# Performance work log

Hardware: AMD Instinct MI355X
Metric: run time of the kernel (lower is better)

Reference implementation:

```python
import jax, jax.numpy as jnp
import numpy as np

B, C, N, D, S = 512, 256, 2048, 64, 3

def setup_inputs() -> dict:
    key = jax.random.key(0)
    k1, k2, k3, k4, k5 = jax.random.split(key, 5)
    controller_output = jax.random.normal(k1, (B, C), dtype=jnp.float32)
    w_prev = jax.random.uniform(k2, (B, N), dtype=jnp.float32)
    w_prev = w_prev / jnp.sum(w_prev, axis=-1, keepdims=True)  # valid attention weighting
    M_t = jax.random.normal(k3, (B, N, D), dtype=jnp.float32)
    emit_len = D + 1 + 1 + S + 1  # read_split sum = 70
    W = jax.random.normal(k4, (C, emit_len), dtype=jnp.float32) * (1.0 / np.sqrt(C))
    b = jax.random.normal(k5, (emit_len,), dtype=jnp.float32) * 0.05
    return {"controller_output": controller_output, "w_t_1": w_prev, "M_t": M_t, "W": W, "b": b}

def reference(controller_output, w_t_1, M_t, W, b):
    # fc_addr: Dense with tanh activation
    fc = jnp.tanh(controller_output @ W + b)  # [B, 70]
    # split per read_split [D,1,1,S,1] and apply emit activations
    k_t = fc[:, :D]                                            # [B, D] (already tanh'd)
    beta_t = jax.nn.softplus(fc[:, D:D + 1])                   # [B, 1] key strength
    g_t = jax.nn.sigmoid(fc[:, D + 1:D + 2])                   # [B, 1] interpolation gate
    s_t = jax.nn.softmax(fc[:, D + 2:D + 2 + S], axis=-1)      # [B, S] shift weighting
    gamma_t = 1.0 + jax.nn.softplus(fc[:, D + 2 + S:D + 3 + S])  # [B, 1] sharpen
    # content addressing: cosine similarity (no epsilon, faithful to source)
    dot = jnp.einsum('bd,bnd->bn', k_t, M_t)                   # [B, N]
    k_mag = jnp.sqrt(jnp.sum(k_t * k_t, axis=-1, keepdims=True))  # [B, 1]
    m_mag = jnp.sqrt(jnp.sum(M_t * M_t, axis=-1))              # [B, N]
    cos = dot / (k_mag * m_mag)
    w_c_t = jax.nn.softmax(beta_t * cos, axis=-1)              # [B, N]
    # interpolation
    w_g_t = g_t * w_c_t + (1.0 - g_t) * w_t_1                  # [B, N]
    # circular convolution shift: sum_i roll(w, i - S//2) * s[:, i]
    w_tilde = jnp.zeros_like(w_g_t)
    for i in range(S):
        w_tilde = w_tilde + jnp.roll(w_g_t, i - S // 2, axis=-1) * s_t[:, i:i + 1]
    # sharpening
    w_raised = jnp.power(w_tilde, gamma_t)
    w_t = w_raised / jnp.sum(w_raised, axis=-1, keepdims=True)  # [B, N]
    # read
    r_t = jnp.einsum('bn,bnd->bd', w_t, M_t)                   # [B, D]
    return (r_t, w_t)
```

## Files before the change

kernel.cpp:

```cpp
#include <hip/hip_runtime.h>
#include <math.h>

constexpr int Bb = 512;
constexpr int Cc = 256;
constexpr int Nn = 2048;
constexpr int Dd = 64;
constexpr int EMIT = Dd + 1 + 1 + 3 + 1;
constexpr int BLOCK = 1024;
constexpr int NW = BLOCK / 64;

__global__ __launch_bounds__(BLOCK, 8)
void ntm_read_head_kernel(const float* __restrict__ co,
                          const float* __restrict__ wprev,
                          const float* __restrict__ M,
                          const float* __restrict__ W,
                          const float* __restrict__ bias,
                          float* __restrict__ out_r,
                          float* __restrict__ out_w)
{
    const int b    = blockIdx.x;
    const int t    = threadIdx.x;
    const int lane = t & 63;
    const int wv   = t >> 6;

    __shared__ __align__(16) float fc[EMIT + 2];
    __shared__ float sc[8];
    __shared__ __align__(16) float zbuf[Nn];
    __shared__ float wpbuf[Nn];
    __shared__ float wtbuf[Nn];
    __shared__ float redA[NW], redB[NW];
    __shared__ float rred[NW][Dd];

    {
        const float* wpv = wprev + (size_t)b * Nn;
        wpbuf[t]        = wpv[t];
        wpbuf[t + 1024] = wpv[t + 1024];
    }

    const float* corow = co + (size_t)b * Cc;
    {
        float* fcp = zbuf;
        if (t < 980) {
            const int j    = t % EMIT;
            const int part = t / EMIT;
            const int c0 = part * 19;
            const int c1 = (c0 + 19 < Cc) ? c0 + 19 : Cc;
            float s = 0.f;
            for (int c = c0; c < c1; ++c)
                s = fmaf(corow[c], W[(size_t)c * EMIT + j], s);
            fcp[part * EMIT + j] = s;
        }
        __syncthreads();
        if (t < EMIT) {
            float s = bias[t];
            #pragma unroll
            for (int w = 0; w < 14; ++w) s += fcp[w * EMIT + t];
            fc[t] = tanhf(s);
        }
    }
    __syncthreads();

    if (t < 64) {
        float kk  = fc[t];
        float ksq = kk * kk;
        #pragma unroll
        for (int o = 1; o < 64; o <<= 1) ksq += __shfl_xor(ksq, o);
        if (t == 0) {
            float kmag  = sqrtf(ksq);
            float beta  = log1pf(expf(fc[Dd]));
            float g     = 1.f / (1.f + expf(-fc[Dd + 1]));
            float f0 = fc[Dd + 2], f1 = fc[Dd + 3], f2 = fc[Dd + 4];
            float mx = fmaxf(f0, fmaxf(f1, f2));
            float e0 = expf(f0 - mx), e1 = expf(f1 - mx), e2 = expf(f2 - mx);
            float ei = 1.f / (e0 + e1 + e2);
            float gamma = 1.f + log1pf(expf(fc[Dd + 5]));
            sc[0] = beta; sc[1] = g;
            sc[2] = e0 * ei; sc[3] = e1 * ei; sc[4] = e2 * ei;
            sc[5] = gamma; sc[6] = 1.f / kmag;
        }
    }
    __syncthreads();

    const size_t mbase = (size_t)b * Nn * Dd;
    float lmax = -3.4e38f;
    {
        const int rg = t >> 2;
        const int p  = t & 3;
        const float beta = sc[0];
        const float kinv = sc[6];
        const float4 k0 = *(const float4*)&fc[p * 16 + 0];
        const float4 k1 = *(const float4*)&fc[p * 16 + 4];
        const float4 k2 = *(const float4*)&fc[p * 16 + 8];
        const float4 k3 = *(const float4*)&fc[p * 16 + 12];
        for (int n0 = 0; n0 < Nn; n0 += BLOCK / 4) {
            const int n = n0 + rg;
            const float4* mr = (const float4*)&M[mbase + (size_t)n * Dd + p * 16];
            const float4 m0 = mr[0];
            const float4 m1 = mr[1];
            const float4 m2 = mr[2];
            const float4 m3 = mr[3];
            float dot = m0.x*k0.x + m0.y*k0.y + m0.z*k0.z + m0.w*k0.w
                      + m1.x*k1.x + m1.y*k1.y + m1.z*k1.z + m1.w*k1.w
                      + m2.x*k2.x + m2.y*k2.y + m2.z*k2.z + m2.w*k2.w
                      + m3.x*k3.x + m3.y*k3.y + m3.z*k3.z + m3.w*k3.w;
            float msq = m0.x*m0.x + m0.y*m0.y + m0.z*m0.z + m0.w*m0.w
                      + m1.x*m1.x + m1.y*m1.y + m1.z*m1.z + m1.w*m1.w
                      + m2.x*m2.x + m2.y*m2.y + m2.z*m2.z + m2.w*m2.w
                      + m3.x*m3.x + m3.y*m3.y + m3.z*m3.z + m3.w*m3.w;
            dot += __shfl_xor(dot, 1);
            msq += __shfl_xor(msq, 1);
            dot += __shfl_xor(dot, 2);
            msq += __shfl_xor(msq, 2);
            if (p == 0) {
                float z = beta * dot * kinv / sqrtf(msq);
                zbuf[n] = z;
                lmax = fmaxf(lmax, z);
            }
        }
    }
    #pragma unroll
    for (int o = 1; o < 64; o <<= 1) lmax = fmaxf(lmax, __shfl_xor(lmax, o));
    if (lane == 0) redA[wv] = lmax;
    __syncthreads();

    float zmax = redA[0];
    #pragma unroll
    for (int w = 1; w < NW; ++w) zmax = fmaxf(zmax, redA[w]);

    float ls = 0.f;
    #pragma unroll
    for (int k = 0; k < 2; ++k) {
        const int n = t + k * 1024;
        float e = __expf(zbuf[n] - zmax);
        zbuf[n] = e;
        ls += e;
    }
    #pragma unroll
    for (int o = 1; o < 64; o <<= 1) ls += __shfl_xor(ls, o);
    if (lane == 0) redB[wv] = ls;
    __syncthreads();

    float Zs = 0.f;
    #pragma unroll
    for (int w = 0; w < NW; ++w) Zs += redB[w];

    float lsum = 0.f;
    {
        const float g  = sc[1];
        const float A  = g / Zs;
        const float Cg = 1.f - g;
        const float s0 = sc[2], s1 = sc[3], s2 = sc[4], gamma = sc[5];
        #pragma unroll
        for (int k = 0; k < 2; ++k) {
            const int n  = t + k * 1024;
            const int np = (n + 1) & (Nn - 1);
            const int nm = (n - 1) & (Nn - 1);
            float ce = s0 * zbuf[np] + s1 * zbuf[n] + s2 * zbuf[nm];
            float cp = s0 * wpbuf[np] + s1 * wpbuf[n] + s2 * wpbuf[nm];
            float wr = __powf(A * ce + Cg * cp, gamma);
            wtbuf[n] = wr;
            lsum += wr;
        }
    }
    #pragma unroll
    for (int o = 1; o < 64; o <<= 1) lsum += __shfl_xor(lsum, o);
    if (lane == 0) redA[wv] = lsum;
    __syncthreads();
    float Ws = 0.f;
    #pragma unroll
    for (int w = 0; w < NW; ++w) Ws += redA[w];

    {
        const float inv = 1.f / Ws;
        float* ow = out_w + (size_t)b * Nn;
        #pragma unroll
        for (int k = 0; k < 2; ++k) {
            const int n = t + k * 1024;
            float v = wtbuf[n] * inv;
            wtbuf[n] = v;
            ow[n] = v;
        }
    }
    __syncthreads();

    {
        const int grp = t >> 4;
        const int dk  = t & 15;
        float4 acc = make_float4(0.f, 0.f, 0.f, 0.f);
        #pragma unroll 4
        for (int n = grp; n < Nn; n += BLOCK / 16) {
            const float w = wtbuf[n];
            const float4 m = *(const float4*)&M[mbase + (size_t)n * Dd + dk * 4];
            acc.x += w * m.x; acc.y += w * m.y;
            acc.z += w * m.z; acc.w += w * m.w;
        }
        #pragma unroll
        for (int o = 16; o < 64; o <<= 1) {
            acc.x += __shfl_xor(acc.x, o);
            acc.y += __shfl_xor(acc.y, o);
            acc.z += __shfl_xor(acc.z, o);
            acc.w += __shfl_xor(acc.w, o);
        }
        if (lane < 16) {
            rred[wv][lane * 4 + 0] = acc.x;
            rred[wv][lane * 4 + 1] = acc.y;
            rred[wv][lane * 4 + 2] = acc.z;
            rred[wv][lane * 4 + 3] = acc.w;
        }
    }
    __syncthreads();
    if (t < Dd) {
        float r = 0.f;
        #pragma unroll
        for (int w = 0; w < NW; ++w) r += rred[w][t];
        out_r[(size_t)b * Dd + t] = r;
    }
}

extern "C" void kernel_launch(void* const* d_in, const int* in_sizes, int n_in,
                              void* d_out, int out_size, void* d_ws, size_t ws_size,
                              hipStream_t stream) {
    const float* co    = (const float*)d_in[0];
    const float* wprev = (const float*)d_in[1];
    const float* M     = (const float*)d_in[2];
    const float* W     = (const float*)d_in[3];
    const float* bias  = (const float*)d_in[4];
    float* out = (float*)d_out;
    float* out_r = out;
    float* out_w = out + (size_t)Bb * Dd;

    ntm_read_head_kernel<<<Bb, BLOCK, 0, stream>>>(co, wprev, M, W, bias, out_r, out_w);
}
```

Baseline: 91.91 us.

## Split fused NTM read head into four kernels staged through workspace

```diff
diff --git a/kernel.cpp b/kernel.cpp
--- a/kernel.cpp
+++ b/kernel.cpp
@@ -6,162 +6,167 @@
 constexpr int Nn = 2048;
 constexpr int Dd = 64;
 constexpr int EMIT = Dd + 1 + 1 + 3 + 1;
-constexpr int BLOCK = 1024;
-constexpr int NW = BLOCK / 64;
-
-__global__ __launch_bounds__(BLOCK, 8)
-void ntm_read_head_kernel(const float* __restrict__ co,
-                          const float* __restrict__ wprev,
-                          const float* __restrict__ M,
-                          const float* __restrict__ W,
-                          const float* __restrict__ bias,
-                          float* __restrict__ out_r,
-                          float* __restrict__ out_w)
-{
-    const int b    = blockIdx.x;
-    const int t    = threadIdx.x;
-    const int lane = t & 63;
-    const int wv   = t >> 6;
-
-    __shared__ __align__(16) float fc[EMIT + 2];
-    __shared__ float sc[8];
-    __shared__ __align__(16) float zbuf[Nn];
+constexpr int NW = 16;
+
+constexpr int FC_STRIDE = 80;
+constexpr int Z_OFF     = Bb * FC_STRIDE;
+constexpr int ZMAX_OFF  = Z_OFF + Bb * Nn;
+
+__global__ __launch_bounds__(256)
+void k0_fc(const float* __restrict__ co, const float* __restrict__ W,
+           const float* __restrict__ bias, float* __restrict__ ws)
+{
+    const int b = blockIdx.x, t = threadIdx.x;
+    __shared__ float part[3][EMIT];
+    __shared__ float fcrow[EMIT];
+    const float* corow = co + (size_t)b * Cc;
+
+    if (t < 210) {
+        const int j = t % EMIT, p = t / EMIT;
+        const int c0 = p * 86, c1 = (p == 2) ? Cc : c0 + 86;
+        float s = 0.f;
+        for (int c = c0; c < c1; ++c)
+            s = fmaf(corow[c], W[(size_t)c * EMIT + j], s);
+        part[p][j] = s;
+    }
+    __syncthreads();
+    if (t < EMIT)
+        fcrow[t] = tanhf(bias[t] + part[0][t] + part[1][t] + part[2][t]);
+    __syncthreads();
+
+    float* wsrow = ws + (size_t)b * FC_STRIDE;
+    if (t < 64) {
+        float kk = fcrow[t];
+        wsrow[t] = kk;
+        float ksq = kk * kk;
+        #pragma unroll
+        for (int o = 1; o < 64; o <<= 1) ksq += __shfl_xor(ksq, o);
+        if (t == 0) {
+            float kinv  = 1.f / sqrtf(ksq);
+            float beta  = log1pf(expf(fcrow[Dd]));
+            float g     = 1.f / (1.f + expf(-fcrow[Dd + 1]));
+            float f0 = fcrow[Dd + 2], f1 = fcrow[Dd + 3], f2 = fcrow[Dd + 4];
+            float mx = fmaxf(f0, fmaxf(f1, f2));
+            float e0 = expf(f0 - mx), e1 = expf(f1 - mx), e2 = expf(f2 - mx);
+            float ei = 1.f / (e0 + e1 + e2);
+            float gamma = 1.f + log1pf(expf(fcrow[Dd + 5]));
+            wsrow[64] = beta; wsrow[65] = g;
+            wsrow[66] = e0 * ei; wsrow[67] = e1 * ei; wsrow[68] = e2 * ei;
+            wsrow[69] = gamma; wsrow[70] = kinv;
+        }
+    }
+}
+
+__global__ __launch_bounds__(1024, 8)
+void k1a_cos(const float* __restrict__ M, float* __restrict__ ws)
+{
+    const int b = blockIdx.x, t = threadIdx.x;
+    const int lane = t & 63, wv = t >> 6;
+    __shared__ __align__(16) float kf[72];
+    __shared__ float redA[NW];
+
+    if (t < 72) kf[t] = ws[(size_t)b * FC_STRIDE + t];
+    __syncthreads();
+
+    const float bk = kf[64] * kf[70];
+    const int rg = t >> 2, p = t & 3;
+    const float4 k0 = *(const float4*)&kf[p * 16 + 0];
+    const float4 k1 = *(const float4*)&kf[p * 16 + 4];
+    const float4 k2 = *(const float4*)&kf[p * 16 + 8];
+    const float4 k3 = *(const float4*)&kf[p * 16 + 12];
+
+    const size_t mbase = (size_t)b * Nn * Dd;
+    float* zrow = ws + Z_OFF + (size_t)b * Nn;
+    float lmax = -3.4e38f;
+
+    #pragma unroll 2
+    for (int n0 = 0; n0 < Nn; n0 += 256) {
+        const int n = n0 + rg;
+        const float4* mr = (const float4*)&M[mbase + (size_t)n * Dd + p * 16];
+        const float4 m0 = mr[0], m1 = mr[1], m2 = mr[2], m3 = mr[3];
+        float dot = m0.x*k0.x + m0.y*k0.y + m0.z*k0.z + m0.w*k0.w
+                  + m1.x*k1.x + m1.y*k1.y + m1.z*k1.z + m1.w*k1.w
+                  + m2.x*k2.x + m2.y*k2.y + m2.z*k2.z + m2.w*k2.w
+                  + m3.x*k3.x + m3.y*k3.y + m3.z*k3.z + m3.w*k3.w;
+        float msq = m0.x*m0.x + m0.y*m0.y + m0.z*m0.z + m0.w*m0.w
+                  + m1.x*m1.x + m1.y*m1.y + m1.z*m1.z + m1.w*m1.w
+                  + m2.x*m2.x + m2.y*m2.y + m2.z*m2.z + m2.w*m2.w
+                  + m3.x*m3.x + m3.y*m3.y + m3.z*m3.z + m3.w*m3.w;
+        dot += __shfl_xor(dot, 1);
+        msq += __shfl_xor(msq, 1);
+        dot += __shfl_xor(dot, 2);
+        msq += __shfl_xor(msq, 2);
+        if (p == 0) {
+            float z = bk * dot / sqrtf(msq);
+            zrow[n] = z;
+            lmax = fmaxf(lmax, z);
+        }
+    }
+    #pragma unroll
+    for (int o = 1; o < 64; o <<= 1) lmax = fmaxf(lmax, __shfl_xor(lmax, o));
+    if (lane == 0) redA[wv] = lmax;
+    __syncthreads();
+    if (t == 0) {
+        float zmax = redA[0];
+        #pragma unroll
+        for (int w = 1; w < NW; ++w) zmax = fmaxf(zmax, redA[w]);
+        ws[ZMAX_OFF + b] = zmax;
+    }
+}
+
+__global__ __launch_bounds__(1024, 8)
+void k1b_weights(const float* __restrict__ wprev, float* __restrict__ ws,
+                 float* __restrict__ out_w)
+{
+    const int b = blockIdx.x, t = threadIdx.x;
+    const int lane = t & 63, wv = t >> 6;
+    __shared__ float zbuf[Nn];
     __shared__ float wpbuf[Nn];
-    __shared__ float wtbuf[Nn];
+    __shared__ float kf[72];
     __shared__ float redA[NW], redB[NW];
-    __shared__ float rred[NW][Dd];
-
+
+    if (t < 72) kf[t] = ws[(size_t)b * FC_STRIDE + t];
     {
         const float* wpv = wprev + (size_t)b * Nn;
         wpbuf[t]        = wpv[t];
         wpbuf[t + 1024] = wpv[t + 1024];
     }
-
-    const float* corow = co + (size_t)b * Cc;
-    {
-        float* fcp = zbuf;
-        if (t < 980) {
-            const int j    = t % EMIT;
-            const int part = t / EMIT;
-            const int c0 = part * 19;
-            const int c1 = (c0 + 19 < Cc) ? c0 + 19 : Cc;
-            float s = 0.f;
-            for (int c = c0; c < c1; ++c)
-                s = fmaf(corow[c], W[(size_t)c * EMIT + j], s);
-            fcp[part * EMIT + j] = s;
-        }
-        __syncthreads();
-        if (t < EMIT) {
-            float s = bias[t];
-            #pragma unroll
-            for (int w = 0; w < 14; ++w) s += fcp[w * EMIT + t];
-            fc[t] = tanhf(s);
-        }
-    }
-    __syncthreads();
-
-    if (t < 64) {
-        float kk  = fc[t];
-        float ksq = kk * kk;
-        #pragma unroll
-        for (int o = 1; o < 64; o <<= 1) ksq += __shfl_xor(ksq, o);
-        if (t == 0) {
-            float kmag  = sqrtf(ksq);
-            float beta  = log1pf(expf(fc[Dd]));
-            float g     = 1.f / (1.f + expf(-fc[Dd + 1]));
-            float f0 = fc[Dd + 2], f1 = fc[Dd + 3], f2 = fc[Dd + 4];
-            float mx = fmaxf(f0, fmaxf(f1, f2));
-            float e0 = expf(f0 - mx), e1 = expf(f1 - mx), e2 = expf(f2 - mx);
-            float ei = 1.f / (e0 + e1 + e2);
-            float gamma = 1.f + log1pf(expf(fc[Dd + 5]));
-            sc[0] = beta; sc[1] = g;
-            sc[2] = e0 * ei; sc[3] = e1 * ei; sc[4] = e2 * ei;
-            sc[5] = gamma; sc[6] = 1.f / kmag;
-        }
-    }
-    __syncthreads();
-
-    const size_t mbase = (size_t)b * Nn * Dd;
-    float lmax = -3.4e38f;
-    {
-        const int rg = t >> 2;
-        const int p  = t & 3;
-        const float beta = sc[0];
-        const float kinv = sc[6];
-        const float4 k0 = *(const float4*)&fc[p * 16 + 0];
-        const float4 k1 = *(const float4*)&fc[p * 16 + 4];
-        const float4 k2 = *(const float4*)&fc[p * 16 + 8];
-        const float4 k3 = *(const float4*)&fc[p * 16 + 12];
-        for (int n0 = 0; n0 < Nn; n0 += BLOCK / 4) {
-            const int n = n0 + rg;
-            const float4* mr = (const float4*)&M[mbase + (size_t)n * Dd + p * 16];
-            const float4 m0 = mr[0];
-            const float4 m1 = mr[1];
-            const float4 m2 = mr[2];
-            const float4 m3 = mr[3];
-            float dot = m0.x*k0.x + m0.y*k0.y + m0.z*k0.z + m0.w*k0.w
-                      + m1.x*k1.x + m1.y*k1.y + m1.z*k1.z + m1.w*k1.w
-                      + m2.x*k2.x + m2.y*k2.y + m2.z*k2.z + m2.w*k2.w
-                      + m3.x*k3.x + m3.y*k3.y + m3.z*k3.z + m3.w*k3.w;
-            float msq = m0.x*m0.x + m0.y*m0.y + m0.z*m0.z + m0.w*m0.w
-                      + m1.x*m1.x + m1.y*m1.y + m1.z*m1.z + m1.w*m1.w
-                      + m2.x*m2.x + m2.y*m2.y + m2.z*m2.z + m2.w*m2.w
-                      + m3.x*m3.x + m3.y*m3.y + m3.z*m3.z + m3.w*m3.w;
-            dot += __shfl_xor(dot, 1);
-            msq += __shfl_xor(msq, 1);
-            dot += __shfl_xor(dot, 2);
-            msq += __shfl_xor(msq, 2);
-            if (p == 0) {
-                float z = beta * dot * kinv / sqrtf(msq);
-                zbuf[n] = z;
-                lmax = fmaxf(lmax, z);
-            }
-        }
-    }
-    #pragma unroll
-    for (int o = 1; o < 64; o <<= 1) lmax = fmaxf(lmax, __shfl_xor(lmax, o));
-    if (lane == 0) redA[wv] = lmax;
-    __syncthreads();
-
-    float zmax = redA[0];
-    #pragma unroll
-    for (int w = 1; w < NW; ++w) zmax = fmaxf(zmax, redA[w]);
+    const float zmax = ws[ZMAX_OFF + b];
+    const float* zrow = ws + Z_OFF + (size_t)b * Nn;
 
     float ls = 0.f;
-    #pragma unroll
-    for (int k = 0; k < 2; ++k) {
-        const int n = t + k * 1024;
-        float e = __expf(zbuf[n] - zmax);
-        zbuf[n] = e;
-        ls += e;
-    }
+    float e0_ = __expf(zrow[t] - zmax);
+    float e1_ = __expf(zrow[t + 1024] - zmax);
+    ls = e0_ + e1_;
+    __syncthreads();
+    zbuf[t] = e0_;
+    zbuf[t + 1024] = e1_;
     #pragma unroll
     for (int o = 1; o < 64; o <<= 1) ls += __shfl_xor(ls, o);
     if (lane == 0) redB[wv] = ls;
     __syncthreads();
-
     float Zs = 0.f;
     #pragma unroll
     for (int w = 0; w < NW; ++w) Zs += redB[w];
 
-    float lsum = 0.f;
+    const float g  = kf[65];
+    const float A  = g / Zs;
+    const float Cg = 1.f - g;
+    const float s0 = kf[66], s1 = kf[67], s2 = kf[68], gamma = kf[69];
+    float wr0, wr1, lsum;
     {
-        const float g  = sc[1];
-        const float A  = g / Zs;
-        const float Cg = 1.f - g;
-        const float s0 = sc[2], s1 = sc[3], s2 = sc[4], gamma = sc[5];
-        #pragma unroll
-        for (int k = 0; k < 2; ++k) {
-            const int n  = t + k * 1024;
-            const int np = (n + 1) & (Nn - 1);
-            const int nm = (n - 1) & (Nn - 1);
-            float ce = s0 * zbuf[np] + s1 * zbuf[n] + s2 * zbuf[nm];
-            float cp = s0 * wpbuf[np] + s1 * wpbuf[n] + s2 * wpbuf[nm];
-            float wr = __powf(A * ce + Cg * cp, gamma);
-            wtbuf[n] = wr;
-            lsum += wr;
-        }
-    }
+        const int n  = t;
+        const int np = (n + 1) & (Nn - 1), nm = (n - 1) & (Nn - 1);
+        wr0 = __powf(A * (s0 * zbuf[np] + s1 * zbuf[n] + s2 * zbuf[nm])
+                   + Cg * (s0 * wpbuf[np] + s1 * wpbuf[n] + s2 * wpbuf[nm]), gamma);
+    }
+    {
+        const int n  = t + 1024;
+        const int np = (n + 1) & (Nn - 1), nm = (n - 1) & (Nn - 1);
+        wr1 = __powf(A * (s0 * zbuf[np] + s1 * zbuf[n] + s2 * zbuf[nm])
+                   + Cg * (s0 * wpbuf[np] + s1 * wpbuf[n] + s2 * wpbuf[nm]), gamma);
+    }
+    lsum = wr0 + wr1;
     #pragma unroll
     for (int o = 1; o < 64; o <<= 1) lsum += __shfl_xor(lsum, o);
     if (lane == 0) redA[wv] = lsum;
@@ -170,43 +175,50 @@
     #pragma unroll
     for (int w = 0; w < NW; ++w) Ws += redA[w];
 
-    {
-        const float inv = 1.f / Ws;
-        float* ow = out_w + (size_t)b * Nn;
-        #pragma unroll
-        for (int k = 0; k < 2; ++k) {
-            const int n = t + k * 1024;
-            float v = wtbuf[n] * inv;
-            wtbuf[n] = v;
-            ow[n] = v;
-        }
-    }
-    __syncthreads();
-
-    {
-        const int grp = t >> 4;
-        const int dk  = t & 15;
-        float4 acc = make_float4(0.f, 0.f, 0.f, 0.f);
-        #pragma unroll 4
-        for (int n = grp; n < Nn; n += BLOCK / 16) {
-            const float w = wtbuf[n];
-            const float4 m = *(const float4*)&M[mbase + (size_t)n * Dd + dk * 4];
-            acc.x += w * m.x; acc.y += w * m.y;
-            acc.z += w * m.z; acc.w += w * m.w;
-        }
-        #pragma unroll
-        for (int o = 16; o < 64; o <<= 1) {
-            acc.x += __shfl_xor(acc.x, o);
-            acc.y += __shfl_xor(acc.y, o);
-            acc.z += __shfl_xor(acc.z, o);
-            acc.w += __shfl_xor(acc.w, o);
-        }
-        if (lane < 16) {
-            rred[wv][lane * 4 + 0] = acc.x;
-            rred[wv][lane * 4 + 1] = acc.y;
-            rred[wv][lane * 4 + 2] = acc.z;
-            rred[wv][lane * 4 + 3] = acc.w;
-        }
+    const float inv = 1.f / Ws;
+    float* ow = out_w + (size_t)b * Nn;
+    ow[t]        = wr0 * inv;
+    ow[t + 1024] = wr1 * inv;
+}
+
+__global__ __launch_bounds__(1024, 8)
+void k2_read(const float* __restrict__ M, const float* __restrict__ out_w,
+             float* __restrict__ out_r)
+{
+    const int b = blockIdx.x, t = threadIdx.x;
+    const int lane = t & 63, wv = t >> 6;
+    __shared__ float wtbuf[Nn];
+    __shared__ float rred[NW][Dd];
+
+    const float* wrow = out_w + (size_t)b * Nn;
+    wtbuf[t]        = wrow[t];
+    wtbuf[t + 1024] = wrow[t + 1024];
+    __syncthreads();
+
+    const size_t mbase = (size_t)b * Nn * Dd;
+    const int grp = t >> 4;
+    const int dk  = t & 15;
+    float4 acc = make_float4(0.f, 0.f, 0.f, 0.f);
+    #pragma unroll 4
+    for (int i = 0; i < Nn / 64; ++i) {
+        const int n = (Nn - 64) - i * 64 + grp;
+        const float w = wtbuf[n];
+        const float4 m = *(const float4*)&M[mbase + (size_t)n * Dd + dk * 4];
+        acc.x += w * m.x; acc.y += w * m.y;
+        acc.z += w * m.z; acc.w += w * m.w;
+    }
+    #pragma unroll
+    for (int o = 16; o < 64; o <<= 1) {
+        acc.x += __shfl_xor(acc.x, o);
+        acc.y += __shfl_xor(acc.y, o);
+        acc.z += __shfl_xor(acc.z, o);
+        acc.w += __shfl_xor(acc.w, o);
+    }
+    if (lane < 16) {
+        rred[wv][lane * 4 + 0] = acc.x;
+        rred[wv][lane * 4 + 1] = acc.y;
+        rred[wv][lane * 4 + 2] = acc.z;
+        rred[wv][lane * 4 + 3] = acc.w;
     }
     __syncthreads();
     if (t < Dd) {
@@ -225,9 +237,13 @@
     const float* M     = (const float*)d_in[2];
     const float* W     = (const float*)d_in[3];
     const float* bias  = (const float*)d_in[4];
-    float* out = (float*)d_out;
+    float* out   = (float*)d_out;
     float* out_r = out;
     float* out_w = out + (size_t)Bb * Dd;
-
-    ntm_read_head_kernel<<<Bb, BLOCK, 0, stream>>>(co, wprev, M, W, bias, out_r, out_w);
-}
+    float* ws    = (float*)d_ws;
+
+    k0_fc      <<<Bb, 256,  0, stream>>>(co, W, bias, ws);
+    k1a_cos    <<<Bb, 1024, 0, stream>>>(M, ws);
+    k1b_weights<<<Bb, 1024, 0, stream>>>(wprev, ws, out_w);
+    k2_read    <<<Bb, 1024, 0, stream>>>(M, out_w, out_r);
+}
```

After: 133.4 us. +45.1%, slower.

## Process two batch rows per block, overlapping row0 read with row1 scoring

Applied to the files above, without the earlier changes.

```diff
diff --git a/kernel.cpp b/kernel.cpp
--- a/kernel.cpp
+++ b/kernel.cpp
@@ -8,8 +8,9 @@
 constexpr int EMIT = Dd + 1 + 1 + 3 + 1;
 constexpr int BLOCK = 1024;
 constexpr int NW = BLOCK / 64;
-
-__global__ __launch_bounds__(BLOCK, 8)
+constexpr int GRID = Bb / 2;
+
+__global__ __launch_bounds__(BLOCK, 4)
 void ntm_read_head_kernel(const float* __restrict__ co,
                           const float* __restrict__ wprev,
                           const float* __restrict__ M,
@@ -18,87 +19,98 @@
                           float* __restrict__ out_r,
                           float* __restrict__ out_w)
 {
-    const int b    = blockIdx.x;
+    const int r0 = blockIdx.x * 2;
+    const int r1 = r0 + 1;
     const int t    = threadIdx.x;
     const int lane = t & 63;
     const int wv   = t >> 6;
 
-    __shared__ __align__(16) float fc[EMIT + 2];
-    __shared__ float sc[8];
-    __shared__ __align__(16) float zbuf[Nn];
-    __shared__ float wpbuf[Nn];
-    __shared__ float wtbuf[Nn];
+    __shared__ __align__(16) float fc0[72], fc1[72];
+    __shared__ __align__(16) float zbuf0[Nn], zbuf1[Nn];
+    __shared__ float wp0[Nn], wp1[Nn];
+    __shared__ float wt0[Nn], wt1[Nn];
     __shared__ float redA[NW], redB[NW];
     __shared__ float rred[NW][Dd];
 
     {
-        const float* wpv = wprev + (size_t)b * Nn;
-        wpbuf[t]        = wpv[t];
-        wpbuf[t + 1024] = wpv[t + 1024];
-    }
-
-    const float* corow = co + (size_t)b * Cc;
-    {
-        float* fcp = zbuf;
+        const float* a = wprev + (size_t)r0 * Nn;
+        const float* b = wprev + (size_t)r1 * Nn;
+        wp0[t] = a[t];  wp0[t + 1024] = a[t + 1024];
+        wp1[t] = b[t];  wp1[t + 1024] = b[t + 1024];
+    }
+
+    {
+        const float* co0 = co + (size_t)r0 * Cc;
+        const float* co1 = co + (size_t)r1 * Cc;
         if (t < 980) {
-            const int j    = t % EMIT;
-            const int part = t / EMIT;
+            const int j = t % EMIT, part = t / EMIT;
             const int c0 = part * 19;
             const int c1 = (c0 + 19 < Cc) ? c0 + 19 : Cc;
-            float s = 0.f;
-            for (int c = c0; c < c1; ++c)
-                s = fmaf(corow[c], W[(size_t)c * EMIT + j], s);
-            fcp[part * EMIT + j] = s;
+            float sA = 0.f, sB = 0.f;
+            for (int c = c0; c < c1; ++c) {
+                const float w = W[(size_t)c * EMIT + j];
+                sA = fmaf(co0[c], w, sA);
+                sB = fmaf(co1[c], w, sB);
+            }
+            zbuf0[part * EMIT + j] = sA;
+            zbuf1[part * EMIT + j] = sB;
         }
         __syncthreads();
         if (t < EMIT) {
             float s = bias[t];
             #pragma unroll
-            for (int w = 0; w < 14; ++w) s += fcp[w * EMIT + t];
-            fc[t] = tanhf(s);
-        }
-    }
-    __syncthreads();
-
-    if (t < 64) {
-        float kk  = fc[t];
+            for (int w = 0; w < 14; ++w) s += zbuf0[w * EMIT + t];
+            fc0[t] = tanhf(s);
+        } else if (t >= 512 && t < 512 + EMIT) {
+            const int j = t - 512;
+            float s = bias[j];
+            #pragma unroll
+            for (int w = 0; w < 14; ++w) s += zbuf1[w * EMIT + j];
+            fc1[j] = tanhf(s);
+        }
+        __syncthreads();
+    }
+
+    if (t < 128) {
+        float* fcX = (t < 64) ? fc0 : fc1;
+        const int l = t & 63;
+        float kk  = fcX[l];
         float ksq = kk * kk;
         #pragma unroll
         for (int o = 1; o < 64; o <<= 1) ksq += __shfl_xor(ksq, o);
-        if (t == 0) {
-            float kmag  = sqrtf(ksq);
-            float beta  = log1pf(expf(fc[Dd]));
-            float g     = 1.f / (1.f + expf(-fc[Dd + 1]));
-            float f0 = fc[Dd + 2], f1 = fc[Dd + 3], f2 = fc[Dd + 4];
+        if (l == 0) {
+            float kinv  = 1.f / sqrtf(ksq);
+            float beta  = log1pf(expf(fcX[Dd]));
+            float g     = 1.f / (1.f + expf(-fcX[Dd + 1]));
+            float f0 = fcX[Dd + 2], f1 = fcX[Dd + 3], f2 = fcX[Dd + 4];
             float mx = fmaxf(f0, fmaxf(f1, f2));
             float e0 = expf(f0 - mx), e1 = expf(f1 - mx), e2 = expf(f2 - mx);
             float ei = 1.f / (e0 + e1 + e2);
-            float gamma = 1.f + log1pf(expf(fc[Dd + 5]));
-            sc[0] = beta; sc[1] = g;
-            sc[2] = e0 * ei; sc[3] = e1 * ei; sc[4] = e2 * ei;
-            sc[5] = gamma; sc[6] = 1.f / kmag;
-        }
-    }
-    __syncthreads();
-
-    const size_t mbase = (size_t)b * Nn * Dd;
-    float lmax = -3.4e38f;
-    {
-        const int rg = t >> 2;
-        const int p  = t & 3;
-        const float beta = sc[0];
-        const float kinv = sc[6];
-        const float4 k0 = *(const float4*)&fc[p * 16 + 0];
-        const float4 k1 = *(const float4*)&fc[p * 16 + 4];
-        const float4 k2 = *(const float4*)&fc[p * 16 + 8];
-        const float4 k3 = *(const float4*)&fc[p * 16 + 12];
-        for (int n0 = 0; n0 < Nn; n0 += BLOCK / 4) {
+            float gamma = 1.f + log1pf(expf(fcX[Dd + 5]));
+            fcX[64] = beta; fcX[65] = g;
+            fcX[66] = e0 * ei; fcX[67] = e1 * ei; fcX[68] = e2 * ei;
+            fcX[69] = gamma; fcX[70] = kinv;
+        }
+    }
+    __syncthreads();
+
+    const size_t mb0 = (size_t)r0 * Nn * Dd;
+    const size_t mb1 = (size_t)r1 * Nn * Dd;
+    const int rg = t >> 2, p = t & 3;
+    const int grp = t >> 4, dk = t & 15;
+
+    float lmax0 = -3.4e38f;
+    {
+        const float bk = fc0[64] * fc0[70];
+        const float4 k0 = *(const float4*)&fc0[p * 16 + 0];
+        const float4 k1 = *(const float4*)&fc0[p * 16 + 4];
+        const float4 k2 = *(const float4*)&fc0[p * 16 + 8];
+        const float4 k3 = *(const float4*)&fc0[p * 16 + 12];
+        #pragma unroll 2
+        for (int n0 = 0; n0 < Nn; n0 += 256) {
             const int n = n0 + rg;
-            const float4* mr = (const float4*)&M[mbase + (size_t)n * Dd + p * 16];
-            const float4 m0 = mr[0];
-            const float4 m1 = mr[1];
-            const float4 m2 = mr[2];
-            const float4 m3 = mr[3];
+            const float4* mr = (const float4*)&M[mb0 + (size_t)n * Dd + p * 16];
+            const float4 m0 = mr[0], m1 = mr[1], m2 = mr[2], m3 = mr[3];
             float dot = m0.x*k0.x + m0.y*k0.y + m0.z*k0.z + m0.w*k0.w
                       + m1.x*k1.x + m1.y*k1.y + m1.z*k1.z + m1.w*k1.w
                       + m2.x*k2.x + m2.y*k2.y + m2.z*k2.z + m2.w*k2.w
@@ -107,90 +119,180 @@
                       + m1.x*m1.x + m1.y*m1.y + m1.z*m1.z + m1.w*m1.w
                       + m2.x*m2.x + m2.y*m2.y + m2.z*m2.z + m2.w*m2.w
                       + m3.x*m3.x + m3.y*m3.y + m3.z*m3.z + m3.w*m3.w;
-            dot += __shfl_xor(dot, 1);
-            msq += __shfl_xor(msq, 1);
-            dot += __shfl_xor(dot, 2);
-            msq += __shfl_xor(msq, 2);
+            dot += __shfl_xor(dot, 1);  msq += __shfl_xor(msq, 1);
+            dot += __shfl_xor(dot, 2);  msq += __shfl_xor(msq, 2);
             if (p == 0) {
-                float z = beta * dot * kinv / sqrtf(msq);
-                zbuf[n] = z;
-                lmax = fmaxf(lmax, z);
+                float z = bk * dot / sqrtf(msq);
+                zbuf0[n] = z;
+                lmax0 = fmaxf(lmax0, z);
             }
         }
     }
     #pragma unroll
-    for (int o = 1; o < 64; o <<= 1) lmax = fmaxf(lmax, __shfl_xor(lmax, o));
-    if (lane == 0) redA[wv] = lmax;
-    __syncthreads();
-
-    float zmax = redA[0];
-    #pragma unroll
-    for (int w = 1; w < NW; ++w) zmax = fmaxf(zmax, redA[w]);
-
-    float ls = 0.f;
-    #pragma unroll
-    for (int k = 0; k < 2; ++k) {
-        const int n = t + k * 1024;
-        float e = __expf(zbuf[n] - zmax);
-        zbuf[n] = e;
-        ls += e;
-    }
-    #pragma unroll
-    for (int o = 1; o < 64; o <<= 1) ls += __shfl_xor(ls, o);
-    if (lane == 0) redB[wv] = ls;
-    __syncthreads();
-
-    float Zs = 0.f;
-    #pragma unroll
-    for (int w = 0; w < NW; ++w) Zs += redB[w];
-
-    float lsum = 0.f;
-    {
-        const float g  = sc[1];
-        const float A  = g / Zs;
-        const float Cg = 1.f - g;
-        const float s0 = sc[2], s1 = sc[3], s2 = sc[4], gamma = sc[5];
-        #pragma unroll
-        for (int k = 0; k < 2; ++k) {
-            const int n  = t + k * 1024;
-            const int np = (n + 1) & (Nn - 1);
-            const int nm = (n - 1) & (Nn - 1);
-            float ce = s0 * zbuf[np] + s1 * zbuf[n] + s2 * zbuf[nm];
-            float cp = s0 * wpbuf[np] + s1 * wpbuf[n] + s2 * wpbuf[nm];
-            float wr = __powf(A * ce + Cg * cp, gamma);
-            wtbuf[n] = wr;
-            lsum += wr;
-        }
-    }
-    #pragma unroll
-    for (int o = 1; o < 64; o <<= 1) lsum += __shfl_xor(lsum, o);
-    if (lane == 0) redA[wv] = lsum;
-    __syncthreads();
-    float Ws = 0.f;
-    #pragma unroll
-    for (int w = 0; w < NW; ++w) Ws += redA[w];
-
-    {
+    for (int o = 1; o < 64; o <<= 1) lmax0 = fmaxf(lmax0, __shfl_xor(lmax0, o));
+    if (lane == 0) redA[wv] = lmax0;
+    __syncthreads();
+    float zmax0 = redA[0];
+    #pragma unroll
+    for (int w = 1; w < NW; ++w) zmax0 = fmaxf(zmax0, redA[w]);
+
+    {
+        float e0 = __expf(zbuf0[t] - zmax0);
+        float e1 = __expf(zbuf0[t + 1024] - zmax0);
+        float ls = e0 + e1;
+        zbuf0[t] = e0; zbuf0[t + 1024] = e1;
+        #pragma unroll
+        for (int o = 1; o < 64; o <<= 1) ls += __shfl_xor(ls, o);
+        if (lane == 0) redB[wv] = ls;
+    }
+    __syncthreads();
+    {
+        float Zs = 0.f;
+        #pragma unroll
+        for (int w = 0; w < NW; ++w) Zs += redB[w];
+        const float g  = fc0[65];
+        const float A  = g / Zs, Cg = 1.f - g;
+        const float s0 = fc0[66], s1 = fc0[67], s2 = fc0[68], gamma = fc0[69];
+        float wr0, wr1;
+        {
+            const int n = t, np = (n + 1) & (Nn - 1), nm = (n - 1) & (Nn - 1);
+            wr0 = __powf(A * (s0 * zbuf0[np] + s1 * zbuf0[n] + s2 * zbuf0[nm])
+                       + Cg * (s0 * wp0[np] + s1 * wp0[n] + s2 * wp0[nm]), gamma);
+        }
+        {
+            const int n = t + 1024, np = (n + 1) & (Nn - 1), nm = (n - 1) & (Nn - 1);
+            wr1 = __powf(A * (s0 * zbuf0[np] + s1 * zbuf0[n] + s2 * zbuf0[nm])
+                       + Cg * (s0 * wp0[np] + s1 * wp0[n] + s2 * wp0[nm]), gamma);
+        }
+        float lsum = wr0 + wr1;
+        #pragma unroll
+        for (int o = 1; o < 64; o <<= 1) lsum += __shfl_xor(lsum, o);
+        if (lane == 0) redA[wv] = lsum;
+        __syncthreads();
+        float Ws = 0.f;
+        #pragma unroll
+        for (int w = 0; w < NW; ++w) Ws += redA[w];
         const float inv = 1.f / Ws;
-        float* ow = out_w + (size_t)b * Nn;
-        #pragma unroll
-        for (int k = 0; k < 2; ++k) {
-            const int n = t + k * 1024;
-            float v = wtbuf[n] * inv;
-            wtbuf[n] = v;
-            ow[n] = v;
-        }
-    }
-    __syncthreads();
-
-    {
-        const int grp = t >> 4;
-        const int dk  = t & 15;
+        float* ow = out_w + (size_t)r0 * Nn;
+        wt0[t] = wr0 * inv;        ow[t] = wr0 * inv;
+        wt0[t + 1024] = wr1 * inv; ow[t + 1024] = wr1 * inv;
+    }
+    __syncthreads();
+
+    float lmax1 = -3.4e38f;
+    float4 acc0 = make_float4(0.f, 0.f, 0.f, 0.f);
+    {
+        const float bk = fc1[64] * fc1[70];
+        const float4 k0 = *(const float4*)&fc1[p * 16 + 0];
+        const float4 k1 = *(const float4*)&fc1[p * 16 + 4];
+        const float4 k2 = *(const float4*)&fc1[p * 16 + 8];
+        const float4 k3 = *(const float4*)&fc1[p * 16 + 12];
+        for (int i = 0; i < 8; ++i) {
+            const int n = i * 256 + rg;
+            const float4* mr = (const float4*)&M[mb1 + (size_t)n * Dd + p * 16];
+            const float4 m0 = mr[0], m1 = mr[1], m2 = mr[2], m3 = mr[3];
+            #pragma unroll
+            for (int jj = 0; jj < 4; ++jj) {
+                const int n2 = i * 256 + jj * 64 + grp;
+                const float w = wt0[n2];
+                const float4 mm = *(const float4*)&M[mb0 + (size_t)n2 * Dd + dk * 4];
+                acc0.x += w * mm.x; acc0.y += w * mm.y;
+                acc0.z += w * mm.z; acc0.w += w * mm.w;
+            }
+            float dot = m0.x*k0.x + m0.y*k0.y + m0.z*k0.z + m0.w*k0.w
+                      + m1.x*k1.x + m1.y*k1.y + m1.z*k1.z + m1.w*k1.w
+                      + m2.x*k2.x + m2.y*k2.y + m2.z*k2.z + m2.w*k2.w
+                      + m3.x*k3.x + m3.y*k3.y + m3.z*k3.z + m3.w*k3.w;
+            float msq = m0.x*m0.x + m0.y*m0.y + m0.z*m0.z + m0.w*m0.w
+                      + m1.x*m1.x + m1.y*m1.y + m1.z*m1.z + m1.w*m1.w
+                      + m2.x*m2.x + m2.y*m2.y + m2.z*m2.z + m2.w*m2.w
+                      + m3.x*m3.x + m3.y*m3.y + m3.z*m3.z + m3.w*m3.w;
+            dot += __shfl_xor(dot, 1);  msq += __shfl_xor(msq, 1);
+            dot += __shfl_xor(dot, 2);  msq += __shfl_xor(msq, 2);
+            if (p == 0) {
+                float z = bk * dot / sqrtf(msq);
+                zbuf1[n] = z;
+                lmax1 = fmaxf(lmax1, z);
+            }
+        }
+    }
+    #pragma unroll
+    for (int o = 1; o < 64; o <<= 1) lmax1 = fmaxf(lmax1, __shfl_xor(lmax1, o));
+    if (lane == 0) redA[wv] = lmax1;
+    #pragma unroll
+    for (int o = 16; o < 64; o <<= 1) {
+        acc0.x += __shfl_xor(acc0.x, o);
+        acc0.y += __shfl_xor(acc0.y, o);
+        acc0.z += __shfl_xor(acc0.z, o);
+        acc0.w += __shfl_xor(acc0.w, o);
+    }
+    if (lane < 16) {
+        rred[wv][lane * 4 + 0] = acc0.x;
+        rred[wv][lane * 4 + 1] = acc0.y;
+        rred[wv][lane * 4 + 2] = acc0.z;
+        rred[wv][lane * 4 + 3] = acc0.w;
+    }
+    __syncthreads();
+    if (t < Dd) {
+        float r = 0.f;
+        #pragma unroll
+        for (int w = 0; w < NW; ++w) r += rred[w][t];
+        out_r[(size_t)r0 * Dd + t] = r;
+    }
+    float zmax1 = redA[0];
+    #pragma unroll
+    for (int w = 1; w < NW; ++w) zmax1 = fmaxf(zmax1, redA[w]);
+
+    {
+        float e0 = __expf(zbuf1[t] - zmax1);
+        float e1 = __expf(zbuf1[t + 1024] - zmax1);
+        float ls = e0 + e1;
+        zbuf1[t] = e0; zbuf1[t + 1024] = e1;
+        #pragma unroll
+        for (int o = 1; o < 64; o <<= 1) ls += __shfl_xor(ls, o);
+        if (lane == 0) redB[wv] = ls;
+    }
+    __syncthreads();
+    {
+        float Zs = 0.f;
+        #pragma unroll
+        for (int w = 0; w < NW; ++w) Zs += redB[w];
+        const float g  = fc1[65];
+        const float A  = g / Zs, Cg = 1.f - g;
+        const float s0 = fc1[66], s1 = fc1[67], s2 = fc1[68], gamma = fc1[69];
+        float wr0, wr1;
+        {
+            const int n = t, np = (n + 1) & (Nn - 1), nm = (n - 1) & (Nn - 1);
+            wr0 = __powf(A * (s0 * zbuf1[np] + s1 * zbuf1[n] + s2 * zbuf1[nm])
+                       + Cg * (s0 * wp1[np] + s1 * wp1[n] + s2 * wp1[nm]), gamma);
+        }
+        {
+            const int n = t + 1024, np = (n + 1) & (Nn - 1), nm = (n - 1) & (Nn - 1);
+            wr1 = __powf(A * (s0 * zbuf1[np] + s1 * zbuf1[n] + s2 * zbuf1[nm])
+                       + Cg * (s0 * wp1[np] + s1 * wp1[n] + s2 * wp1[nm]), gamma);
+        }
+        float lsum = wr0 + wr1;
+        #pragma unroll
+        for (int o = 1; o < 64; o <<= 1) lsum += __shfl_xor(lsum, o);
+        if (lane == 0) redA[wv] = lsum;
+        __syncthreads();
+        float Ws = 0.f;
+        #pragma unroll
+        for (int w = 0; w < NW; ++w) Ws += redA[w];
+        const float inv = 1.f / Ws;
+        float* ow = out_w + (size_t)r1 * Nn;
+        wt1[t] = wr0 * inv;        ow[t] = wr0 * inv;
+        wt1[t + 1024] = wr1 * inv; ow[t + 1024] = wr1 * inv;
+    }
+    __syncthreads();
+
+    {
         float4 acc = make_float4(0.f, 0.f, 0.f, 0.f);
         #pragma unroll 4
-        for (int n = grp; n < Nn; n += BLOCK / 16) {
-            const float w = wtbuf[n];
-            const float4 m = *(const float4*)&M[mbase + (size_t)n * Dd + dk * 4];
+        for (int i = 0; i < Nn / 64; ++i) {
+            const int n = (Nn - 64) - i * 64 + grp;
+            const float w = wt1[n];
+            const float4 m = *(const float4*)&M[mb1 + (size_t)n * Dd + dk * 4];
             acc.x += w * m.x; acc.y += w * m.y;
             acc.z += w * m.z; acc.w += w * m.w;
         }
@@ -213,7 +315,7 @@
         float r = 0.f;
         #pragma unroll
         for (int w = 0; w < NW; ++w) r += rred[w][t];
-        out_r[(size_t)b * Dd + t] = r;
+        out_r[(size_t)r1 * Dd + t] = r;
     }
 }
 
@@ -225,9 +327,9 @@
     const float* M     = (const float*)d_in[2];
     const float* W     = (const float*)d_in[3];
     const float* bias  = (const float*)d_in[4];
-    float* out = (float*)d_out;
+    float* out   = (float*)d_out;
     float* out_r = out;
     float* out_w = out + (size_t)Bb * Dd;
 
-    ntm_read_head_kernel<<<Bb, BLOCK, 0, stream>>>(co, wprev, M, W, bias, out_r, out_w);
+    ntm_read_head_kernel<<<GRID, BLOCK, 0, stream>>>(co, wprev, M, W, bias, out_r, out_w);
 }
```

After: 131.8 us. +43.5%, slower.

## Split read-head kernel into weight and read kernels, reverse M traversal

Applied to the files above, without the earlier changes.

```diff
diff --git a/kernel.cpp b/kernel.cpp
--- a/kernel.cpp
+++ b/kernel.cpp
@@ -10,26 +10,22 @@
 constexpr int NW = BLOCK / 64;
 
 __global__ __launch_bounds__(BLOCK, 8)
-void ntm_read_head_kernel(const float* __restrict__ co,
-                          const float* __restrict__ wprev,
-                          const float* __restrict__ M,
-                          const float* __restrict__ W,
-                          const float* __restrict__ bias,
-                          float* __restrict__ out_r,
-                          float* __restrict__ out_w)
+void kA_weights(const float* __restrict__ co,
+                const float* __restrict__ wprev,
+                const float* __restrict__ M,
+                const float* __restrict__ W,
+                const float* __restrict__ bias,
+                float* __restrict__ out_w)
 {
     const int b    = blockIdx.x;
     const int t    = threadIdx.x;
     const int lane = t & 63;
     const int wv   = t >> 6;
 
-    __shared__ __align__(16) float fc[EMIT + 2];
-    __shared__ float sc[8];
+    __shared__ __align__(16) float fc[72];
     __shared__ __align__(16) float zbuf[Nn];
     __shared__ float wpbuf[Nn];
-    __shared__ float wtbuf[Nn];
     __shared__ float redA[NW], redB[NW];
-    __shared__ float rred[NW][Dd];
 
     {
         const float* wpv = wprev + (size_t)b * Nn;
@@ -39,22 +35,20 @@
 
     const float* corow = co + (size_t)b * Cc;
     {
-        float* fcp = zbuf;
         if (t < 980) {
-            const int j    = t % EMIT;
-            const int part = t / EMIT;
+            const int j = t % EMIT, part = t / EMIT;
             const int c0 = part * 19;
             const int c1 = (c0 + 19 < Cc) ? c0 + 19 : Cc;
             float s = 0.f;
             for (int c = c0; c < c1; ++c)
                 s = fmaf(corow[c], W[(size_t)c * EMIT + j], s);
-            fcp[part * EMIT + j] = s;
+            zbuf[part * EMIT + j] = s;
         }
         __syncthreads();
         if (t < EMIT) {
             float s = bias[t];
             #pragma unroll
-            for (int w = 0; w < 14; ++w) s += fcp[w * EMIT + t];
+            for (int w = 0; w < 14; ++w) s += zbuf[w * EMIT + t];
             fc[t] = tanhf(s);
         }
     }
@@ -66,7 +60,7 @@
         #pragma unroll
         for (int o = 1; o < 64; o <<= 1) ksq += __shfl_xor(ksq, o);
         if (t == 0) {
-            float kmag  = sqrtf(ksq);
+            float kinv  = 1.f / sqrtf(ksq);
             float beta  = log1pf(expf(fc[Dd]));
             float g     = 1.f / (1.f + expf(-fc[Dd + 1]));
             float f0 = fc[Dd + 2], f1 = fc[Dd + 3], f2 = fc[Dd + 4];
@@ -74,9 +68,9 @@
             float e0 = expf(f0 - mx), e1 = expf(f1 - mx), e2 = expf(f2 - mx);
             float ei = 1.f / (e0 + e1 + e2);
             float gamma = 1.f + log1pf(expf(fc[Dd + 5]));
-            sc[0] = beta; sc[1] = g;
-            sc[2] = e0 * ei; sc[3] = e1 * ei; sc[4] = e2 * ei;
-            sc[5] = gamma; sc[6] = 1.f / kmag;
+            fc[64] = beta; fc[65] = g;
+            fc[66] = e0 * ei; fc[67] = e1 * ei; fc[68] = e2 * ei;
+            fc[69] = gamma; fc[70] = kinv;
         }
     }
     __syncthreads();
@@ -84,21 +78,17 @@
     const size_t mbase = (size_t)b * Nn * Dd;
     float lmax = -3.4e38f;
     {
-        const int rg = t >> 2;
-        const int p  = t & 3;
-        const float beta = sc[0];
-        const float kinv = sc[6];
+        const int rg = t >> 2, p = t & 3;
+        const float bk = fc[64] * fc[70];
         const float4 k0 = *(const float4*)&fc[p * 16 + 0];
         const float4 k1 = *(const float4*)&fc[p * 16 + 4];
         const float4 k2 = *(const float4*)&fc[p * 16 + 8];
         const float4 k3 = *(const float4*)&fc[p * 16 + 12];
-        for (int n0 = 0; n0 < Nn; n0 += BLOCK / 4) {
+        #pragma unroll 2
+        for (int n0 = 0; n0 < Nn; n0 += 256) {
             const int n = n0 + rg;
             const float4* mr = (const float4*)&M[mbase + (size_t)n * Dd + p * 16];
-            const float4 m0 = mr[0];
-            const float4 m1 = mr[1];
-            const float4 m2 = mr[2];
-            const float4 m3 = mr[3];
+            const float4 m0 = mr[0], m1 = mr[1], m2 = mr[2], m3 = mr[3];
             float dot = m0.x*k0.x + m0.y*k0.y + m0.z*k0.z + m0.w*k0.w
                       + m1.x*k1.x + m1.y*k1.y + m1.z*k1.z + m1.w*k1.w
                       + m2.x*k2.x + m2.y*k2.y + m2.z*k2.z + m2.w*k2.w
@@ -107,12 +97,10 @@
                       + m1.x*m1.x + m1.y*m1.y + m1.z*m1.z + m1.w*m1.w
                       + m2.x*m2.x + m2.y*m2.y + m2.z*m2.z + m2.w*m2.w
                       + m3.x*m3.x + m3.y*m3.y + m3.z*m3.z + m3.w*m3.w;
-            dot += __shfl_xor(dot, 1);
-            msq += __shfl_xor(msq, 1);
-            dot += __shfl_xor(dot, 2);
-            msq += __shfl_xor(msq, 2);
+            dot += __shfl_xor(dot, 1);  msq += __shfl_xor(msq, 1);
+            dot += __shfl_xor(dot, 2);  msq += __shfl_xor(msq, 2);
             if (p == 0) {
-                float z = beta * dot * kinv / sqrtf(msq);
+                float z = bk * dot / sqrtf(msq);
                 zbuf[n] = z;
                 lmax = fmaxf(lmax, z);
             }
@@ -122,46 +110,40 @@
     for (int o = 1; o < 64; o <<= 1) lmax = fmaxf(lmax, __shfl_xor(lmax, o));
     if (lane == 0) redA[wv] = lmax;
     __syncthreads();
-
     float zmax = redA[0];
     #pragma unroll
     for (int w = 1; w < NW; ++w) zmax = fmaxf(zmax, redA[w]);
 
-    float ls = 0.f;
-    #pragma unroll
-    for (int k = 0; k < 2; ++k) {
-        const int n = t + k * 1024;
-        float e = __expf(zbuf[n] - zmax);
-        zbuf[n] = e;
-        ls += e;
+    float ls;
+    {
+        float e0 = __expf(zbuf[t] - zmax);
+        float e1 = __expf(zbuf[t + 1024] - zmax);
+        ls = e0 + e1;
+        zbuf[t] = e0; zbuf[t + 1024] = e1;
     }
     #pragma unroll
     for (int o = 1; o < 64; o <<= 1) ls += __shfl_xor(ls, o);
     if (lane == 0) redB[wv] = ls;
     __syncthreads();
-
     float Zs = 0.f;
     #pragma unroll
     for (int w = 0; w < NW; ++w) Zs += redB[w];
 
-    float lsum = 0.f;
-    {
-        const float g  = sc[1];
-        const float A  = g / Zs;
-        const float Cg = 1.f - g;
-        const float s0 = sc[2], s1 = sc[3], s2 = sc[4], gamma = sc[5];
-        #pragma unroll
-        for (int k = 0; k < 2; ++k) {
-            const int n  = t + k * 1024;
-            const int np = (n + 1) & (Nn - 1);
-            const int nm = (n - 1) & (Nn - 1);
-            float ce = s0 * zbuf[np] + s1 * zbuf[n] + s2 * zbuf[nm];
-            float cp = s0 * wpbuf[np] + s1 * wpbuf[n] + s2 * wpbuf[nm];
-            float wr = __powf(A * ce + Cg * cp, gamma);
-            wtbuf[n] = wr;
-            lsum += wr;
-        }
-    }
+    const float g  = fc[65];
+    const float A  = g / Zs, Cg = 1.f - g;
+    const float s0 = fc[66], s1 = fc[67], s2 = fc[68], gamma = fc[69];
+    float wr0, wr1;
+    {
+        const int n = t, np = (n + 1) & (Nn - 1), nm = (n - 1) & (Nn - 1);
+        wr0 = __powf(A * (s0 * zbuf[np] + s1 * zbuf[n] + s2 * zbuf[nm])
+                   + Cg * (s0 * wpbuf[np] + s1 * wpbuf[n] + s2 * wpbuf[nm]), gamma);
+    }
+    {
+        const int n = t + 1024, np = (n + 1) & (Nn - 1), nm = (n - 1) & (Nn - 1);
+        wr1 = __powf(A * (s0 * zbuf[np] + s1 * zbuf[n] + s2 * zbuf[nm])
+                   + Cg * (s0 * wpbuf[np] + s1 * wpbuf[n] + s2 * wpbuf[nm]), gamma);
+    }
+    float lsum = wr0 + wr1;
     #pragma unroll
     for (int o = 1; o < 64; o <<= 1) lsum += __shfl_xor(lsum, o);
     if (lane == 0) redA[wv] = lsum;
@@ -170,43 +152,50 @@
     #pragma unroll
     for (int w = 0; w < NW; ++w) Ws += redA[w];
 
-    {
-        const float inv = 1.f / Ws;
-        float* ow = out_w + (size_t)b * Nn;
-        #pragma unroll
-        for (int k = 0; k < 2; ++k) {
-            const int n = t + k * 1024;
-            float v = wtbuf[n] * inv;
-            wtbuf[n] = v;
-            ow[n] = v;
-        }
-    }
-    __syncthreads();
-
-    {
-        const int grp = t >> 4;
-        const int dk  = t & 15;
-        float4 acc = make_float4(0.f, 0.f, 0.f, 0.f);
-        #pragma unroll 4
-        for (int n = grp; n < Nn; n += BLOCK / 16) {
-            const float w = wtbuf[n];
-            const float4 m = *(const float4*)&M[mbase + (size_t)n * Dd + dk * 4];
-            acc.x += w * m.x; acc.y += w * m.y;
-            acc.z += w * m.z; acc.w += w * m.w;
-        }
-        #pragma unroll
-        for (int o = 16; o < 64; o <<= 1) {
-            acc.x += __shfl_xor(acc.x, o);
-            acc.y += __shfl_xor(acc.y, o);
-            acc.z += __shfl_xor(acc.z, o);
-            acc.w += __shfl_xor(acc.w, o);
-        }
-        if (lane < 16) {
-            rred[wv][lane * 4 + 0] = acc.x;
-            rred[wv][lane * 4 + 1] = acc.y;
-            rred[wv][lane * 4 + 2] = acc.z;
-            rred[wv][lane * 4 + 3] = acc.w;
-        }
+    const float inv = 1.f / Ws;
+    float* ow = out_w + (size_t)b * Nn;
+    ow[t]        = wr0 * inv;
+    ow[t + 1024] = wr1 * inv;
+}
+
+__global__ __launch_bounds__(BLOCK, 8)
+void kB_read(const float* __restrict__ M, const float* __restrict__ out_w,
+             float* __restrict__ out_r)
+{
+    const int b = blockIdx.x, t = threadIdx.x;
+    const int lane = t & 63, wv = t >> 6;
+    __shared__ float wtbuf[Nn];
+    __shared__ float rred[NW][Dd];
+
+    const float* wrow = out_w + (size_t)b * Nn;
+    wtbuf[t]        = wrow[t];
+    wtbuf[t + 1024] = wrow[t + 1024];
+    __syncthreads();
+
+    const size_t mbase = (size_t)b * Nn * Dd;
+    const int grp = t >> 4;
+    const int dk  = t & 15;
+    float4 acc = make_float4(0.f, 0.f, 0.f, 0.f);
+    #pragma unroll 4
+    for (int i = 0; i < Nn / 64; ++i) {
+        const int n = (Nn - 64) - i * 64 + grp;
+        const float w = wtbuf[n];
+        const float4 m = *(const float4*)&M[mbase + (size_t)n * Dd + dk * 4];
+        acc.x += w * m.x; acc.y += w * m.y;
+        acc.z += w * m.z; acc.w += w * m.w;
+    }
+    #pragma unroll
+    for (int o = 16; o < 64; o <<= 1) {
+        acc.x += __shfl_xor(acc.x, o);
+        acc.y += __shfl_xor(acc.y, o);
+        acc.z += __shfl_xor(acc.z, o);
+        acc.w += __shfl_xor(acc.w, o);
+    }
+    if (lane < 16) {
+        rred[wv][lane * 4 + 0] = acc.x;
+        rred[wv][lane * 4 + 1] = acc.y;
+        rred[wv][lane * 4 + 2] = acc.z;
+        rred[wv][lane * 4 + 3] = acc.w;
     }
     __syncthreads();
     if (t < Dd) {
@@ -225,9 +214,10 @@
     const float* M     = (const float*)d_in[2];
     const float* W     = (const float*)d_in[3];
     const float* bias  = (const float*)d_in[4];
-    float* out = (float*)d_out;
+    float* out   = (float*)d_out;
     float* out_r = out;
     float* out_w = out + (size_t)Bb * Dd;
 
-    ntm_read_head_kernel<<<Bb, BLOCK, 0, stream>>>(co, wprev, M, W, bias, out_r, out_w);
+    kA_weights<<<Bb, BLOCK, 0, stream>>>(co, wprev, M, W, bias, out_w);
+    kB_read   <<<Bb, BLOCK, 0, stream>>>(M, out_w, out_r);
 }
```

Result: slower. 100.5 us (+9.4%).
